# Performance work log

Measured on AMD Instinct MI355X. Metric: run time of the kernel, lower is better.

The kernel has to match this reference:

```python
import jax, jax.numpy as jnp
import numpy as np

CH = 512
COND = 1280
HEADS = 8
GROUPS = CH // 8
EPS = 1e-5


def conv2d(x, w, b, pad):
    y = jax.lax.conv_general_dilated(
        x, w, window_strides=(1, 1), padding=[(pad, pad), (pad, pad)],
        dimension_numbers=('NCHW', 'OIHW', 'NCHW'))
    return y + b[None, :, None, None]


def group_norm(x, gamma, beta, groups, eps=EPS):
    b, c, h, w = x.shape
    xg = x.reshape(b, groups, c // groups, h, w)
    mu = xg.mean(axis=(2, 3, 4), keepdims=True)
    var = xg.var(axis=(2, 3, 4), keepdims=True)
    xn = ((xg - mu) * jax.lax.rsqrt(var + eps)).reshape(b, c, h, w)
    return xn * gamma[None, :, None, None] + beta[None, :, None, None]


def setup_inputs() -> dict:
    key = jax.random.key(0)
    ks = jax.random.split(key, 20)
    s = 0.05
    inp = {
        'x': jax.random.normal(ks[0], (8, CH, 32, 32), jnp.float32),
        'conditioning': jax.random.normal(ks[1], (8, COND), jnp.float32),
        # ResBlock params
        'c1w': jax.random.normal(ks[2], (CH, CH, 3, 3), jnp.float32) * s,
        'c1b': jnp.zeros((CH,), jnp.float32),
        'g1w': jnp.ones((CH,), jnp.float32),
        'g1b': jnp.zeros((CH,), jnp.float32),
        'c2w': jax.random.normal(ks[3], (CH, CH, 3, 3), jnp.float32) * s,
        'c2b': jnp.zeros((CH,), jnp.float32),
        'g2w': jnp.ones((CH,), jnp.float32),
        'g2b': jnp.zeros((CH,), jnp.float32),
        'cpw': jax.random.normal(ks[4], (CH, COND), jnp.float32) * s,
        'cpb': jnp.zeros((CH,), jnp.float32),
        'rpw': jax.random.normal(ks[5], (CH, CH, 1, 1), jnp.float32) * s,
        'rpb': jnp.zeros((CH,), jnp.float32),
        # Attention params (1x1 convs)
        'qw': jax.random.normal(ks[6], (CH, CH, 1, 1), jnp.float32) * s,
        'qb': jnp.zeros((CH,), jnp.float32),
        'kw': jax.random.normal(ks[7], (CH, CH, 1, 1), jnp.float32) * s,
        'kb': jnp.zeros((CH,), jnp.float32),
        'vw': jax.random.normal(ks[8], (CH, CH, 1, 1), jnp.float32) * s,
        'vb': jnp.zeros((CH,), jnp.float32),
        'ow': jax.random.normal(ks[9], (CH, CH, 1, 1), jnp.float32) * s,
        'ob': jnp.zeros((CH,), jnp.float32),
    }
    return inp


def reference(x, conditioning, c1w, c1b, g1w, g1b, c2w, c2b, g2w, g2b,
              cpw, cpb, rpw, rpb, qw, qb, kw, kb, vw, vb, ow, ob):
    # --- ResBlock ---
    residual = conv2d(x, rpw, rpb, 0)
    h = conv2d(x, c1w, c1b, 1)
    h = group_norm(h, g1w, g1b, GROUPS)
    h = jax.nn.silu(h)
    h = conv2d(h, c2w, c2b, 1)
    h = group_norm(h, g2w, g2b, GROUPS)
    cond = conditioning @ cpw.T + cpb  # [B, C]
    h = h * (1.0 + cond[:, :, None, None]) + residual

    # --- SpatialSelfAttention ---
    b, c, hh, ww = h.shape
    d = c // HEADS
    scale = d ** (-0.5)
    q = conv2d(h, qw, qb, 0).reshape(b, HEADS, d, hh * ww)
    k = conv2d(h, kw, kb, 0).reshape(b, HEADS, d, hh * ww)
    v = conv2d(h, vw, vb, 0).reshape(b, HEADS, d, hh * ww)
    attn = jnp.einsum('bhdn,bhdm->bhnm', q, k) * scale  # [B,H,N,N]
    attn = jax.nn.softmax(attn, axis=-1)
    out = jnp.einsum('bhnm,bhdm->bhdn', attn, v).reshape(b, c, hh, ww)
    return conv2d(out, ow, ob, 0) + h
```

## Files before the change

### kernel.cpp

```cpp
#include <hip/hip_runtime.h>
#include <hip/hip_bf16.h>

typedef unsigned short u16;
typedef __attribute__((ext_vector_type(8))) short bf8;
typedef __attribute__((ext_vector_type(4))) short bf4;
typedef __attribute__((ext_vector_type(4))) float f32x4;

#define CH_ 512
#define NSP 1024
#define NB 8
#define CONDDIM 1280
#define NGROUP 64
#define HEADS_ 8
#define HD 64
#define PR 34
#define PPB (PR*PR)
#define QSCALE 0.18033688011112042f

#define VWAIT(N) asm volatile("s_waitcnt vmcnt(" #N ")" ::: "memory")
#define SCHEDB __builtin_amdgcn_sched_barrier(0)
#define BARRIER do { SCHEDB; __builtin_amdgcn_s_barrier(); SCHEDB; } while (0)

__device__ __forceinline__ u16 f2bf(float f) {
  union { float f; unsigned u; } v; v.f = f;
  unsigned u = v.u;
  return (u16)((u + 0x7fffu + ((u >> 16) & 1u)) >> 16);
}

__device__ __forceinline__ unsigned cvt_pk_bf16(float lo, float hi) {
  unsigned r;
  asm volatile("v_cvt_pk_bf16_f32 %0, %1, %2" : "=v"(r) : "v"(lo), "v"(hi));
  return r;
}

__device__ __forceinline__ f32x4 mfma_bf16(bf8 a, bf8 b, f32x4 c) {
  return __builtin_amdgcn_mfma_f32_16x16x32_bf16(a, b, c, 0, 0, 0);
}

__device__ __forceinline__ void gload16(const void* g, void* l) {
  __builtin_amdgcn_global_load_lds((const __attribute__((address_space(1))) void*)g,
                                   (__attribute__((address_space(3))) void*)l, 16, 0, 0);
}


__global__ __launch_bounds__(1024) void pack_x_kernel(const float* __restrict__ x, u16* __restrict__ xp) {
  __shared__ float t[32][33];
  int b = blockIdx.z;
  int c0 = blockIdx.y * 32, p0 = blockIdx.x * 32;
  int tx = threadIdx.x & 31, ty = threadIdx.x >> 5;
  t[ty][tx] = x[((size_t)b * CH_ + c0 + ty) * NSP + p0 + tx];
  __syncthreads();
  int p = p0 + ty;
  int y = p >> 5, xc = p & 31;
  xp[((size_t)b * PPB + (size_t)(y + 1) * PR + xc + 1) * CH_ + c0 + tx] = f2bf(t[tx][ty]);
}

__global__ __launch_bounds__(256) void border_zero_kernel(u16* __restrict__ a, u16* __restrict__ b) {
  int id = blockIdx.x * 256 + threadIdx.x;
  if (id >= NB * 132 * 64) return;
  int ch8 = id & 63;
  int rest = id >> 6;
  int bidx = rest % 132;
  int bb = rest / 132;
  int r, c;
  if (bidx < 34)       { r = 0;          c = bidx; }
  else if (bidx < 68)  { r = 33;         c = bidx - 34; }
  else if (bidx < 100) { r = bidx - 67;  c = 0; }
  else                 { r = bidx - 99;  c = 33; }
  size_t off = ((size_t)bb * PPB + (size_t)r * PR + c) * CH_ + ch8 * 8;
  const bf8 z = {0, 0, 0, 0, 0, 0, 0, 0};
  *(bf8*)(a + off) = z;
  *(bf8*)(b + off) = z;
}

__global__ __launch_bounds__(256) void pack_w3_kernel(const float* __restrict__ w, u16* __restrict__ wp) {
  int id = blockIdx.x * 256 + threadIdx.x;
  if (id >= 9 * 64 * CH_) return;
  int co = id & (CH_ - 1);
  int cib = (id >> 9) & 63;
  int t = id >> 15;
  int dy = t / 3, dx = t % 3;
  bf8 v;
#pragma unroll
  for (int j = 0; j < 8; j++) {
    int ci = cib * 8 + j;
    v[j] = (short)f2bf(w[(((size_t)co * CH_ + ci) * 3 + dy) * 3 + dx]);
  }
  *(bf8*)(wp + ((size_t)(t * 64 + cib) * CH_ + co) * 8) = v;
}

__global__ __launch_bounds__(256) void pack_w1_kernel(const float* __restrict__ w, u16* __restrict__ wp) {
  int id = blockIdx.x * 256 + threadIdx.x;
  if (id >= 64 * CH_) return;
  int co = id & (CH_ - 1);
  int cib = id >> 9;
  bf8 v;
#pragma unroll
  for (int j = 0; j < 8; j++) v[j] = (short)f2bf(w[(size_t)co * CH_ + cib * 8 + j]);
  *(bf8*)(wp + ((size_t)cib * CH_ + co) * 8) = v;
}

__global__ __launch_bounds__(256) void cond_kernel(const float* __restrict__ cd, const float* __restrict__ cpw,
                                                   const float* __restrict__ cpb, float* __restrict__ cond) {
  int b = blockIdx.y;
  int c = blockIdx.x * 4 + (threadIdx.x >> 6);
  int lane = threadIdx.x & 63;
  const float* wrow = cpw + (size_t)c * CONDDIM;
  const float* crow = cd + (size_t)b * CONDDIM;
  float s = 0.f;
  for (int i = lane; i < CONDDIM; i += 64) s += crow[i] * wrow[i];
#pragma unroll
  for (int m = 32; m > 0; m >>= 1) s += __shfl_xor(s, m, 64);
  if (lane == 0) cond[b * CH_ + c] = s + cpb[c];
}

template <int TAPS, int PIN, int EPI>
__global__ __launch_bounds__(256, TAPS == 9 ? 4 : 3) void conv_kernel(
    const u16* __restrict__ in, const u16* __restrict__ wp, const float* __restrict__ bias,
    float* __restrict__ outf, const float* __restrict__ addf,
    u16* __restrict__ o0, u16* __restrict__ o1, u16* __restrict__ o2,
    const float* __restrict__ b0, const float* __restrict__ b1, const float* __restrict__ b2) {
  constexpr int LDSZ = (TAPS == 9) ? (2 * 14336 + 3 * 4096) : (4 * 8192 + 4 * 4096);
  __shared__ char lds[LDSZ];
  char* ldsA = lds;
  char* ldsB = lds + ((TAPS == 9) ? 2 * 14336 : 4 * 8192);

  const int b = blockIdx.z;
  int seg = 0, coy = blockIdx.y;
  if constexpr (EPI == 5) { seg = coy >> 3; coy &= 7; }
  const int co0 = coy * 64;
  const int p0 = blockIdx.x * 128;
  const int tid = threadIdx.x;
  const int lane = tid & 63, wid = tid >> 6;
  const int wv = wid >> 1, wc = wid & 1;
  const int l15 = lane & 15, lhi = lane >> 4;

  const char* aSrc;
  if constexpr (TAPS == 9) {
    aSrc = (const char*)in + ((size_t)b * PPB + (size_t)blockIdx.x * 4 * PR) * 1024;
  } else if constexpr (PIN) {
    aSrc = (const char*)in + (size_t)b * PPB * 1024;
  } else {
    aSrc = (const char*)in + ((size_t)b * NSP + p0) * 1024;
  }
  const char* bSrc = (const char*)wp + (size_t)((EPI == 5) ? seg * 524288 : 0) + co0 * 16;

  const int pB = ((tid >> 6) * 512 + (tid & 63)) * 16;
  int pA0, pA1, pA3 = 0;
  if constexpr (TAPS == 9) {
    pA0 = ((tid >> 2) << 10) + ((tid & 3) << 4);
    pA3 = ((192 + ((tid & 127) >> 2)) << 10) + ((tid & 3) << 4);
    pA1 = 0;
  } else {
    int a0 = (tid >> 2), a1 = 64 + (tid >> 2);
    if constexpr (PIN) {
      int pp0 = p0 + a0, pp1 = p0 + a1;
      int g0 = ((pp0 >> 5) + 1) * PR + (pp0 & 31) + 1;
      int g1 = ((pp1 >> 5) + 1) * PR + (pp1 & 31) + 1;
      pA0 = (g0 << 10) + ((tid & 3) << 4);
      pA1 = (g1 << 10) + ((tid & 3) << 4);
    } else {
      pA0 = (a0 << 10) + ((tid & 3) << 4);
      pA1 = (a1 << 10) + ((tid & 3) << 4);
    }
  }

  const int aAddr = (TAPS == 9) ? ((wv * 68 + l15) * 64 + lhi * 16)
                                : ((wv * 64 + l15) * 64 + lhi * 16);
  const int bAddr = (lhi * 64 + wc * 32 + l15) * 16;

  f32x4 acc[4][2];
#pragma unroll
  for (int m = 0; m < 4; m++)
#pragma unroll
    for (int n = 0; n < 2; n++) acc[m][n] = {0.f, 0.f, 0.f, 0.f};

  if constexpr (TAPS == 9) {
    gload16(aSrc + pA0,          ldsA + (wid << 10));
    gload16(aSrc + pA0 + 65536,  ldsA + 4096 + (wid << 10));
    gload16(aSrc + pA0 + 131072, ldsA + 8192 + (wid << 10));
    gload16(aSrc + pA3,          ldsA + 12288 + ((wid & 1) << 10));
    gload16(bSrc + pB,           ldsB + (wid << 10));
    gload16(bSrc + 524288 + pB,  ldsB + 4096 + (wid << 10));
    VWAIT(1);
    BARRIER;

#define PH9(KC, T, AS) do {                                                             \
    constexpr int DT = ((T) / 3) * 34 + ((T) % 3);                                      \
    const int kcn_ = ((KC) < 15) ? (KC) + 1 : 15;                                       \
    { const int kb_ = ((T) >= 7) ? kcn_ : (KC);                                         \
      constexpr int TB = ((T) + 2) % 9;                                                 \
      gload16(bSrc + (size_t)(TB * 64 + kb_ * 4) * 8192 + pB,                           \
              ldsB + (((T) + 2) % 3) * 4096 + (wid << 10)); }                           \
    if constexpr ((T) >= 4 && (T) < 7)                                                  \
      gload16(aSrc + kcn_ * 64 + pA0 + ((T) - 4) * 65536,                               \
              ldsA + (1 - (AS)) * 14336 + ((T) - 4) * 4096 + (wid << 10));              \
    if constexpr ((T) == 7)                                                             \
      gload16(aSrc + kcn_ * 64 + pA3,                                                   \
              ldsA + (1 - (AS)) * 14336 + 12288 + ((wid & 1) << 10));                   \
    SCHEDB;                                                                             \
    bf8 af0 = *(const bf8*)(ldsA + (AS) * 14336 + DT * 64 + 0    + aAddr);              \
    bf8 af1 = *(const bf8*)(ldsA + (AS) * 14336 + DT * 64 + 1024 + aAddr);              \
    bf8 af2 = *(const bf8*)(ldsA + (AS) * 14336 + DT * 64 + 2176 + aAddr);              \
    bf8 af3 = *(const bf8*)(ldsA + (AS) * 14336 + DT * 64 + 3200 + aAddr);              \
    bf8 bq0 = *(const bf8*)(ldsB + ((T) % 3) * 4096 + 0   + bAddr);                     \
    bf8 bq1 = *(const bf8*)(ldsB + ((T) % 3) * 4096 + 256 + bAddr);                     \
    __builtin_amdgcn_s_setprio(1);                                                      \
    acc[0][0] = mfma_bf16(af0, bq0, acc[0][0]);                                         \
    acc[0][1] = mfma_bf16(af0, bq1, acc[0][1]);                                         \
    acc[1][0] = mfma_bf16(af1, bq0, acc[1][0]);                                         \
    acc[1][1] = mfma_bf16(af1, bq1, acc[1][1]);                                         \
    acc[2][0] = mfma_bf16(af2, bq0, acc[2][0]);                                         \
    acc[2][1] = mfma_bf16(af2, bq1, acc[2][1]);                                         \
    acc[3][0] = mfma_bf16(af3, bq0, acc[3][0]);                                         \
    acc[3][1] = mfma_bf16(af3, bq1, acc[3][1]);                                         \
    __builtin_amdgcn_s_setprio(0);                                                      \
    if constexpr ((T) >= 4 && (T) <= 7) { VWAIT(2); } else { VWAIT(1); }                \
    BARRIER;                                                                            \
  } while (0)

    for (int kc2 = 0; kc2 < 8; kc2++) {
      PH9(kc2 * 2, 0, 0); PH9(kc2 * 2, 1, 0); PH9(kc2 * 2, 2, 0);
      PH9(kc2 * 2, 3, 0); PH9(kc2 * 2, 4, 0); PH9(kc2 * 2, 5, 0);
      PH9(kc2 * 2, 6, 0); PH9(kc2 * 2, 7, 0); PH9(kc2 * 2, 8, 0);
      PH9(kc2 * 2 + 1, 0, 1); PH9(kc2 * 2 + 1, 1, 1); PH9(kc2 * 2 + 1, 2, 1);
      PH9(kc2 * 2 + 1, 3, 1); PH9(kc2 * 2 + 1, 4, 1); PH9(kc2 * 2 + 1, 5, 1);
      PH9(kc2 * 2 + 1, 6, 1); PH9(kc2 * 2 + 1, 7, 1); PH9(kc2 * 2 + 1, 8, 1);
    }
#undef PH9
  } else {
    gload16(aSrc + pA0,         ldsA + (wid << 10));
    gload16(aSrc + pA1,         ldsA + 4096 + (wid << 10));
    gload16(bSrc + pB,          ldsB + (wid << 10));
    gload16(aSrc + 64 + pA0,    ldsA + 8192 + (wid << 10));
    gload16(aSrc + 64 + pA1,    ldsA + 8192 + 4096 + (wid << 10));
    gload16(bSrc + 32768 + pB,  ldsB + 4096 + (wid << 10));
    VWAIT(3);
    BARRIER;

#define PH1(KC, S) do {                                                                 \
    constexpr int S2 = ((S) + 2) & 3;                                                   \
    const int kcn_ = ((KC) + 2 < 16) ? (KC) + 2 : 15;                                   \
    gload16(bSrc + (size_t)kcn_ * 32768 + pB, ldsB + S2 * 4096 + (wid << 10));          \
    gload16(aSrc + kcn_ * 64 + pA0, ldsA + S2 * 8192 + (wid << 10));                    \
    gload16(aSrc + kcn_ * 64 + pA1, ldsA + S2 * 8192 + 4096 + (wid << 10));             \
    SCHEDB;                                                                             \
    bf8 af0 = *(const bf8*)(ldsA + (S) * 8192 + 0    + aAddr);                          \
    bf8 af1 = *(const bf8*)(ldsA + (S) * 8192 + 1024 + aAddr);                          \
    bf8 af2 = *(const bf8*)(ldsA + (S) * 8192 + 2048 + aAddr);                          \
    bf8 af3 = *(const bf8*)(ldsA + (S) * 8192 + 3072 + aAddr);                          \
    bf8 bq0 = *(const bf8*)(ldsB + (S) * 4096 + 0   + bAddr);                           \
    bf8 bq1 = *(const bf8*)(ldsB + (S) * 4096 + 256 + bAddr);                           \
    __builtin_amdgcn_s_setprio(1);                                                      \
    acc[0][0] = mfma_bf16(af0, bq0, acc[0][0]);                                         \
    acc[0][1] = mfma_bf16(af0, bq1, acc[0][1]);                                         \
    acc[1][0] = mfma_bf16(af1, bq0, acc[1][0]);                                         \
    acc[1][1] = mfma_bf16(af1, bq1, acc[1][1]);                                         \
    acc[2][0] = mfma_bf16(af2, bq0, acc[2][0]);                                         \
    acc[2][1] = mfma_bf16(af2, bq1, acc[2][1]);                                         \
    acc[3][0] = mfma_bf16(af3, bq0, acc[3][0]);                                         \
    acc[3][1] = mfma_bf16(af3, bq1, acc[3][1]);                                         \
    __builtin_amdgcn_s_setprio(0);                                                      \
    VWAIT(3);                                                                           \
    BARRIER;                                                                            \
  } while (0)

    for (int kc4 = 0; kc4 < 4; kc4++) {
      PH1(kc4 * 4 + 0, 0); PH1(kc4 * 4 + 1, 1); PH1(kc4 * 4 + 2, 2); PH1(kc4 * 4 + 3, 3);
    }
#undef PH1
  }

  VWAIT(0);

#pragma unroll
  for (int m = 0; m < 4; m++) {
    int pbase = p0 + wv * 64 + m * 16 + lhi * 4;
#pragma unroll
    for (int n = 0; n < 2; n++) {
      int co = co0 + wc * 32 + n * 16 + l15;
      if constexpr (EPI == 0) {
        float bv = bias[co];
#pragma unroll
        for (int r = 0; r < 4; r++)
          outf[((size_t)b * NSP + pbase + r) * CH_ + co] = acc[m][n][r] + bv;
      } else if constexpr (EPI == 2) {
        float bv = bias[co];
        f32x4 v;
#pragma unroll
        for (int r = 0; r < 4; r++)
          v[r] = acc[m][n][r] + bv + addf[((size_t)b * NSP + pbase + r) * CH_ + co];
        *(f32x4*)(outf + ((size_t)b * CH_ + co) * NSP + pbase) = v;
      } else {
        if (seg == 0) {
          float bv = b0[co];
#pragma unroll
          for (int r = 0; r < 4; r++)
            o0[((size_t)b * NSP + pbase + r) * CH_ + co] = f2bf((acc[m][n][r] + bv) * QSCALE);
        } else if (seg == 1) {
          float bv = b1[co];
#pragma unroll
          for (int r = 0; r < 4; r++)
            o1[((size_t)b * NSP + pbase + r) * CH_ + co] = f2bf(acc[m][n][r] + bv);
        } else {
          float bv = b2[co];
          union { bf4 v; unsigned long long u; } pk4;
#pragma unroll
          for (int r = 0; r < 4; r++) pk4.v[r] = (short)f2bf(acc[m][n][r] + bv);
          *(unsigned long long*)(o2 + ((size_t)b * CH_ + co) * NSP + pbase) = pk4.u;
        }
      }
    }
  }
}

template <int MODE>
__global__ __launch_bounds__(256) void gn_kernel(
    const float* __restrict__ in, const float* __restrict__ gw, const float* __restrict__ gb,
    const float* __restrict__ cond, const float* __restrict__ resid,
    float* __restrict__ outf, u16* __restrict__ outb) {
  int b = blockIdx.y, g = blockIdx.x;
  int tid = threadIdx.x;
  int c = g * 8 + (tid & 7);
  int prow = tid >> 3;
  const float* base = in + (size_t)b * NSP * CH_ + c;
  float v[32];
  float s = 0.f, ss = 0.f;
#pragma unroll
  for (int i = 0; i < 32; i++) {
    v[i] = base[(size_t)(prow + i * 32) * CH_];
    s += v[i]; ss += v[i] * v[i];
  }
  __shared__ float rs[256], rss[256];
  rs[tid] = s; rss[tid] = ss;
  __syncthreads();
  for (int off = 128; off > 0; off >>= 1) {
    if (tid < off) { rs[tid] += rs[tid + off]; rss[tid] += rss[tid + off]; }
    __syncthreads();
  }
  float mean = rs[0] * (1.f / 8192.f);
  float var = rss[0] * (1.f / 8192.f) - mean * mean;
  float inv = rsqrtf(var + 1e-5f);
  float gamma = gw[c], beta = gb[c];
  float cm = 0.f;
  if (MODE == 1) cm = 1.f + cond[b * CH_ + c];
#pragma unroll
  for (int i = 0; i < 32; i++) {
    int p = prow + i * 32;
    float y = (v[i] - mean) * inv * gamma + beta;
    if (MODE == 0) {
      float sg = 1.f / (1.f + __expf(-y));
      int yy = p >> 5, xc = p & 31;
      outb[((size_t)b * PPB + (size_t)(yy + 1) * PR + xc + 1) * CH_ + c] = f2bf(y * sg);
    } else {
      size_t idx = ((size_t)b * NSP + p) * CH_ + c;
      float z = y * cm + resid[idx];
      outf[idx] = z;
      outb[idx] = f2bf(z);
    }
  }
}

__global__ __launch_bounds__(256) void attn_kernel(const u16* __restrict__ q, const u16* __restrict__ k,
                                                   const u16* __restrict__ vT, u16* __restrict__ ao) {
  int bid = blockIdx.x;
  int swz = (bid & 7) * 64 + (bid >> 3);
  int b = swz >> 6;
  int head = (swz >> 3) & 7;
  int qt = swz & 7;
  int tid = threadIdx.x, lane = tid & 63, wid = tid >> 6;
  int l15 = lane & 15, lhi = lane >> 4;
  int cb = head * HD;
  int q0 = qt * 128 + wid * 32;

  const char* qp = (const char*)(q + (size_t)b * NSP * CH_ + cb);
  const char* kp = (const char*)(k + (size_t)b * NSP * CH_ + cb);
  const char* vp = (const char*)(vT + ((size_t)b * CH_ + cb) * NSP);

  __shared__ u16 Ksh[3][64 * 64];
  __shared__ u16 Vsh[3][64 * 64];

  bf8 aq[2][2];
#pragma unroll
  for (int qh = 0; qh < 2; qh++)
#pragma unroll
    for (int ks = 0; ks < 2; ks++)
      aq[qh][ks] = *(const bf8*)(qp + ((size_t)(q0 + qh * 16 + l15) * CH_ + ks * 32 + lhi * 8) * 2);

  f32x4 o[2][4];
  float mrow[2], lpart[2];
#pragma unroll
  for (int qh = 0; qh < 2; qh++) {
    mrow[qh] = -1e30f; lpart[qh] = 0.f;
#pragma unroll
    for (int n = 0; n < 4; n++) o[qh][n] = {0.f, 0.f, 0.f, 0.f};
  }

  auto stage = [&](int kt, int buf) {
#pragma unroll
    for (int t = 0; t < 2; t++) {
      int i = wid * 2 + t;
      int chunk = i * 64 + lane;
      int r = chunk >> 3, c = chunk & 7;
      gload16(kp + (size_t)(kt * 64 + r) * 1024 + (size_t)((c ^ (r & 7)) * 16),
              (char*)Ksh[buf] + i * 1024);
    }
#pragma unroll
    for (int t = 0; t < 2; t++) {
      int i = wid * 2 + t;
      int chunk = i * 64 + lane;
      int r = chunk >> 3, c = chunk & 7;
      gload16(vp + (size_t)r * 2048 + (size_t)(kt * 128) + (size_t)((c ^ (r & 7)) * 16),
              (char*)Vsh[buf] + i * 1024);
    }
  };

  stage(0, 0);
  stage(1, 1);

  int cB = 0, sB = 2;
  for (int kt = 0; kt < 16; ++kt) {
    if (kt < 15) { VWAIT(4); } else { VWAIT(0); }
    BARRIER;
    if (kt < 14) stage(kt + 2, sB);
    const char* Kb = (const char*)Ksh[0] + cB * 8192;
    const char* Vb = (const char*)Vsh[0] + cB * 8192;

    f32x4 sacc[2][4];
#pragma unroll
    for (int qh = 0; qh < 2; qh++)
#pragma unroll
      for (int kf = 0; kf < 4; kf++) sacc[qh][kf] = {0.f, 0.f, 0.f, 0.f};

#pragma unroll
    for (int kf = 0; kf < 4; kf++) {
      bf8 ak[2];
#pragma unroll
      for (int ks = 0; ks < 2; ks++)
        ak[ks] = *(const bf8*)(Kb + (size_t)(kf * 16 + l15) * 128 + (((ks * 4 + lhi) ^ (l15 & 7)) * 16));
#pragma unroll
      for (int qh = 0; qh < 2; qh++)
#pragma unroll
        for (int ks = 0; ks < 2; ks++)
          sacc[qh][kf] = mfma_bf16(ak[ks], aq[qh][ks], sacc[qh][kf]);
    }

    unsigned pk[2][4][2];
#pragma unroll
    for (int qh = 0; qh < 2; qh++) {
      float m0 = fmaxf(fmaxf(sacc[qh][0][0], sacc[qh][0][1]), fmaxf(sacc[qh][0][2], sacc[qh][0][3]));
      float m1 = fmaxf(fmaxf(sacc[qh][1][0], sacc[qh][1][1]), fmaxf(sacc[qh][1][2], sacc[qh][1][3]));
      float m2 = fmaxf(fmaxf(sacc[qh][2][0], sacc[qh][2][1]), fmaxf(sacc[qh][2][2], sacc[qh][2][3]));
      float m3 = fmaxf(fmaxf(sacc[qh][3][0], sacc[qh][3][1]), fmaxf(sacc[qh][3][2], sacc[qh][3][3]));
      float pml = fmaxf(fmaxf(m0, m1), fmaxf(m2, m3));
      if (__any(pml > mrow[qh] + 8.f)) {
        float pm = fmaxf(pml, __shfl_xor(pml, 16, 64));
        pm = fmaxf(pm, __shfl_xor(pm, 32, 64));
        float mn = fmaxf(mrow[qh], pm);
        float corr = exp2f(mrow[qh] - mn);
        mrow[qh] = mn;
        lpart[qh] *= corr;
        float corr_o[4];
#pragma unroll
        for (int r = 0; r < 4; r++) corr_o[r] = __shfl(corr, lhi * 4 + r, 64);
#pragma unroll
        for (int n = 0; n < 4; n++)
#pragma unroll
          for (int r = 0; r < 4; r++) o[qh][n][r] *= corr_o[r];
      }
      float rsum = 0.f;
#pragma unroll
      for (int kf = 0; kf < 4; kf++) {
        f32x4 pv;
#pragma unroll
        for (int r = 0; r < 4; r++) {
          pv[r] = exp2f(sacc[qh][kf][r] - mrow[qh]);
          rsum += pv[r];
        }
        pk[qh][kf][0] = cvt_pk_bf16(pv[0], pv[1]);
        pk[qh][kf][1] = cvt_pk_bf16(pv[2], pv[3]);
      }
      lpart[qh] += rsum;
    }

#pragma unroll
    for (int g = 0; g < 2; g++) {
      union { bf8 v8; unsigned u[4]; } ap[2];
#pragma unroll
      for (int qh = 0; qh < 2; qh++) {
        ap[qh].u[0] = pk[qh][2 * g][0];
        ap[qh].u[1] = pk[qh][2 * g][1];
        ap[qh].u[2] = pk[qh][2 * g + 1][0];
        ap[qh].u[3] = pk[qh][2 * g + 1][1];
      }
#pragma unroll
      for (int nf2 = 0; nf2 < 4; nf2++) {
        int row = nf2 * 16 + l15;
        int c0 = 4 * g + (lhi >> 1);
        union { bf8 v8; bf4 v4[2]; } bv;
        bv.v4[0] = *(const bf4*)(Vb + (size_t)row * 128 + ((c0 ^ (l15 & 7)) * 16) + (lhi & 1) * 8);
        bv.v4[1] = *(const bf4*)(Vb + (size_t)row * 128 + (((c0 + 2) ^ (l15 & 7)) * 16) + (lhi & 1) * 8);
#pragma unroll
        for (int qh = 0; qh < 2; qh++)
          o[qh][nf2] = mfma_bf16(ap[qh].v8, bv.v8, o[qh][nf2]);
      }
    }

    cB = (cB == 2) ? 0 : cB + 1;
    sB = (sB == 2) ? 0 : sB + 1;
  }

#pragma unroll
  for (int qh = 0; qh < 2; qh++) {
    float lrow = lpart[qh];
    lrow += __shfl_xor(lrow, 16, 64);
    lrow += __shfl_xor(lrow, 32, 64);
    float linv[4];
#pragma unroll
    for (int r = 0; r < 4; r++) linv[r] = 1.f / __shfl(lrow, lhi * 4 + r, 64);
#pragma unroll
    for (int nf2 = 0; nf2 < 4; nf2++)
#pragma unroll
      for (int r = 0; r < 4; r++) {
        float val = o[qh][nf2][r] * linv[r];
        ao[((size_t)b * NSP + q0 + qh * 16 + lhi * 4 + r) * CH_ + cb + nf2 * 16 + l15] = f2bf(val);
      }
  }
}


extern "C" void kernel_launch(void* const* d_in, const int* in_sizes, int n_in,
                              void* d_out, int out_size, void* d_ws, size_t ws_size,
                              hipStream_t stream) {
  const float* x    = (const float*)d_in[0];
  const float* cnd  = (const float*)d_in[1];
  const float* c1w  = (const float*)d_in[2];
  const float* c1b  = (const float*)d_in[3];
  const float* g1w  = (const float*)d_in[4];
  const float* g1b  = (const float*)d_in[5];
  const float* c2w  = (const float*)d_in[6];
  const float* c2b  = (const float*)d_in[7];
  const float* g2w  = (const float*)d_in[8];
  const float* g2b  = (const float*)d_in[9];
  const float* cpw  = (const float*)d_in[10];
  const float* cpb  = (const float*)d_in[11];
  const float* rpw  = (const float*)d_in[12];
  const float* rpb  = (const float*)d_in[13];
  const float* qw   = (const float*)d_in[14];
  const float* qb   = (const float*)d_in[15];
  const float* kw   = (const float*)d_in[16];
  const float* kb   = (const float*)d_in[17];
  const float* vw   = (const float*)d_in[18];
  const float* vb   = (const float*)d_in[19];
  const float* ow   = (const float*)d_in[20];
  const float* ob   = (const float*)d_in[21];
  float* out = (float*)d_out;

  char* ws = (char*)d_ws;
  size_t off = 0;
  auto alloc = [&](size_t bytes) -> char* {
    char* p = ws + off;
    off = (off + bytes + 255) & ~(size_t)255;
    return p;
  };
  const size_t ACT_F = (size_t)NB * NSP * CH_ * 4;
  const size_t ACT_B = (size_t)NB * NSP * CH_ * 2;
  const size_t PAD_B = (size_t)NB * PPB * CH_ * 2;

  u16* xp    = (u16*)alloc(PAD_B);
  u16* h1p   = (u16*)alloc(PAD_B);
  u16* w1p   = (u16*)alloc((size_t)9 * CH_ * CH_ * 2);
  u16* w2p   = (u16*)alloc((size_t)9 * CH_ * CH_ * 2);
  u16* wrp   = (u16*)alloc((size_t)CH_ * CH_ * 2);
  u16* wqkv  = (u16*)alloc((size_t)3 * CH_ * CH_ * 2);
  u16* wop   = (u16*)alloc((size_t)CH_ * CH_ * 2);
  float* cndv = (float*)alloc((size_t)NB * CH_ * 4);
  float* resid = (float*)alloc(ACT_F);
  float* h12  = (float*)alloc(ACT_F);
  u16* hb    = (u16*)alloc(ACT_B);
  u16* qbuf  = (u16*)alloc(ACT_B);
  u16* kbuf  = (u16*)alloc(ACT_B);
  u16* vTb   = (u16*)alloc(ACT_B);
  u16* aob   = (u16*)alloc(ACT_B);
  if (off > ws_size) return;

  dim3 tgrid(NSP / 32, CH_ / 32, NB);
  border_zero_kernel<<<(NB * 132 * 64 + 255) / 256, 256, 0, stream>>>(xp, h1p);
  pack_x_kernel<<<tgrid, 1024, 0, stream>>>(x, xp);
  pack_w3_kernel<<<(9 * 64 * CH_ + 255) / 256, 256, 0, stream>>>(c1w, w1p);
  pack_w3_kernel<<<(9 * 64 * CH_ + 255) / 256, 256, 0, stream>>>(c2w, w2p);
  pack_w1_kernel<<<(64 * CH_) / 256, 256, 0, stream>>>(rpw, wrp);
  pack_w1_kernel<<<(64 * CH_) / 256, 256, 0, stream>>>(qw, wqkv);
  pack_w1_kernel<<<(64 * CH_) / 256, 256, 0, stream>>>(kw, wqkv + (size_t)CH_ * CH_);
  pack_w1_kernel<<<(64 * CH_) / 256, 256, 0, stream>>>(vw, wqkv + (size_t)2 * CH_ * CH_);
  pack_w1_kernel<<<(64 * CH_) / 256, 256, 0, stream>>>(ow, wop);
  cond_kernel<<<dim3(CH_ / 4, NB), 256, 0, stream>>>(cnd, cpw, cpb, cndv);

  dim3 ggrid(NSP / 128, CH_ / 64, NB);
  dim3 qgrid(NSP / 128, 3 * CH_ / 64, NB);
  conv_kernel<9, 1, 0><<<ggrid, 256, 0, stream>>>(xp, w1p, c1b, h12, nullptr,
                                                  nullptr, nullptr, nullptr, nullptr, nullptr, nullptr);
  conv_kernel<1, 1, 0><<<ggrid, 256, 0, stream>>>(xp, wrp, rpb, resid, nullptr,
                                                  nullptr, nullptr, nullptr, nullptr, nullptr, nullptr);
  gn_kernel<0><<<dim3(NGROUP, NB), 256, 0, stream>>>(h12, g1w, g1b, nullptr, nullptr, nullptr, h1p);
  conv_kernel<9, 1, 0><<<ggrid, 256, 0, stream>>>(h1p, w2p, c2b, h12, nullptr,
                                                  nullptr, nullptr, nullptr, nullptr, nullptr, nullptr);
  gn_kernel<1><<<dim3(NGROUP, NB), 256, 0, stream>>>(h12, g2w, g2b, cndv, resid, h12, hb);
  conv_kernel<1, 0, 5><<<qgrid, 256, 0, stream>>>(hb, wqkv, nullptr, nullptr, nullptr,
                                                  qbuf, kbuf, vTb, qb, kb, vb);
  attn_kernel<<<512, 256, 0, stream>>>(qbuf, kbuf, vTb, aob);
  conv_kernel<1, 0, 2><<<ggrid, 256, 0, stream>>>(aob, wop, ob, out, h12,
                                                  nullptr, nullptr, nullptr, nullptr, nullptr, nullptr);
}
```

Baseline: 265.2 us.

## Restructure 3x3 conv pipeline per row, software-pipeline attention, batch weight packing

The 3x3 conv main loop now stages the weights for a whole kernel row of three taps per phase, with double-buffered B tiles. This cuts the number of barriers per K chunk from nine to three, at the cost of more LDS and lower occupancy (launch bounds drop from 4 to 3). The attention kernel is software-pipelined so the next tile's QK^T overlaps the current softmax and PV, and the V layout is permuted so each lane reads one 16-byte vector instead of two 8-byte ones. The seven weight-packing launches are merged into two using a grid y dimension.

```diff
diff --git a/kernel.cpp b/kernel.cpp
--- a/kernel.cpp
+++ b/kernel.cpp
@@ -2,6 +2,7 @@
 #include <hip/hip_bf16.h>
 
 typedef unsigned short u16;
+typedef unsigned long long u64;
 typedef __attribute__((ext_vector_type(8))) short bf8;
 typedef __attribute__((ext_vector_type(4))) short bf4;
 typedef __attribute__((ext_vector_type(4))) float f32x4;
@@ -73,9 +74,12 @@
   *(bf8*)(b + off) = z;
 }
 
-__global__ __launch_bounds__(256) void pack_w3_kernel(const float* __restrict__ w, u16* __restrict__ wp) {
+__global__ __launch_bounds__(256) void pack_w3_kernel(const float* __restrict__ wA, const float* __restrict__ wB,
+                                                      u16* __restrict__ dA, u16* __restrict__ dB) {
   int id = blockIdx.x * 256 + threadIdx.x;
   if (id >= 9 * 64 * CH_) return;
+  const float* w = blockIdx.y ? wB : wA;
+  u16* wp = blockIdx.y ? dB : dA;
   int co = id & (CH_ - 1);
   int cib = (id >> 9) & 63;
   int t = id >> 15;
@@ -89,9 +93,21 @@
   *(bf8*)(wp + ((size_t)(t * 64 + cib) * CH_ + co) * 8) = v;
 }
 
-__global__ __launch_bounds__(256) void pack_w1_kernel(const float* __restrict__ w, u16* __restrict__ wp) {
+__global__ __launch_bounds__(256) void pack_w1_kernel(
+    const float* __restrict__ s0, const float* __restrict__ s1, const float* __restrict__ s2,
+    const float* __restrict__ s3, const float* __restrict__ s4,
+    u16* __restrict__ d0, u16* __restrict__ d1, u16* __restrict__ d2,
+    u16* __restrict__ d3, u16* __restrict__ d4) {
   int id = blockIdx.x * 256 + threadIdx.x;
   if (id >= 64 * CH_) return;
+  const float* w; u16* wp;
+  switch (blockIdx.y) {
+    case 0: w = s0; wp = d0; break;
+    case 1: w = s1; wp = d1; break;
+    case 2: w = s2; wp = d2; break;
+    case 3: w = s3; wp = d3; break;
+    default: w = s4; wp = d4; break;
+  }
   int co = id & (CH_ - 1);
   int cib = id >> 9;
   bf8 v;
@@ -115,12 +131,12 @@
 }
 
 template <int TAPS, int PIN, int EPI>
-__global__ __launch_bounds__(256, TAPS == 9 ? 4 : 3) void conv_kernel(
+__global__ __launch_bounds__(256, 3) void conv_kernel(
     const u16* __restrict__ in, const u16* __restrict__ wp, const float* __restrict__ bias,
     float* __restrict__ outf, const float* __restrict__ addf,
     u16* __restrict__ o0, u16* __restrict__ o1, u16* __restrict__ o2,
     const float* __restrict__ b0, const float* __restrict__ b1, const float* __restrict__ b2) {
-  constexpr int LDSZ = (TAPS == 9) ? (2 * 14336 + 3 * 4096) : (4 * 8192 + 4 * 4096);
+  constexpr int LDSZ = (TAPS == 9) ? (2 * 14336 + 2 * 12288) : (4 * 8192 + 4 * 4096);
   __shared__ char lds[LDSZ];
   char* ldsA = lds;
   char* ldsB = lds + ((TAPS == 9) ? 2 * 14336 : 4 * 8192);
@@ -182,52 +198,63 @@
     gload16(aSrc + pA3,          ldsA + 12288 + ((wid & 1) << 10));
     gload16(bSrc + pB,           ldsB + (wid << 10));
     gload16(bSrc + 524288 + pB,  ldsB + 4096 + (wid << 10));
-    VWAIT(1);
+    gload16(bSrc + 1048576 + pB, ldsB + 8192 + (wid << 10));
+    VWAIT(0);
     BARRIER;
 
-#define PH9(KC, T, AS) do {                                                             \
-    constexpr int DT = ((T) / 3) * 34 + ((T) % 3);                                      \
+#define PH3(KC, T, AS, H) do {                                                          \
     const int kcn_ = ((KC) < 15) ? (KC) + 1 : 15;                                       \
-    { const int kb_ = ((T) >= 7) ? kcn_ : (KC);                                         \
-      constexpr int TB = ((T) + 2) % 9;                                                 \
-      gload16(bSrc + (size_t)(TB * 64 + kb_ * 4) * 8192 + pB,                           \
-              ldsB + (((T) + 2) % 3) * 4096 + (wid << 10)); }                           \
-    if constexpr ((T) >= 4 && (T) < 7)                                                  \
-      gload16(aSrc + kcn_ * 64 + pA0 + ((T) - 4) * 65536,                               \
-              ldsA + (1 - (AS)) * 14336 + ((T) - 4) * 4096 + (wid << 10));              \
-    if constexpr ((T) == 7)                                                             \
-      gload16(aSrc + kcn_ * 64 + pA3,                                                   \
-              ldsA + (1 - (AS)) * 14336 + 12288 + ((wid & 1) << 10));                   \
+    { const int kb_ = ((T) == 2) ? kcn_ : (KC);                                         \
+      const int tn_ = 3 * (((T) + 1) % 3);                                              \
+      gload16(bSrc + (size_t)((tn_ + 0) * 64 + kb_ * 4) * 8192 + pB,                    \
+              ldsB + (1 - (H)) * 12288 + (wid << 10));                                  \
+      gload16(bSrc + (size_t)((tn_ + 1) * 64 + kb_ * 4) * 8192 + pB,                    \
+              ldsB + (1 - (H)) * 12288 + 4096 + (wid << 10));                           \
+      gload16(bSrc + (size_t)((tn_ + 2) * 64 + kb_ * 4) * 8192 + pB,                    \
+              ldsB + (1 - (H)) * 12288 + 8192 + (wid << 10)); }                         \
+    if constexpr ((T) == 0) {                                                           \
+      gload16(aSrc + kcn_ * 64 + pA0,         ldsA + (1-(AS))*14336 + (wid << 10));     \
+      gload16(aSrc + kcn_ * 64 + pA0 + 65536, ldsA + (1-(AS))*14336 + 4096 + (wid<<10));\
+    }                                                                                   \
+    if constexpr ((T) == 1)                                                             \
+      gload16(aSrc + kcn_ * 64 + pA0 + 131072, ldsA + (1-(AS))*14336 + 8192 + (wid<<10));\
+    if constexpr ((T) == 2)                                                             \
+      gload16(aSrc + kcn_ * 64 + pA3, ldsA + (1-(AS))*14336 + 12288 + ((wid&1)<<10));   \
     SCHEDB;                                                                             \
-    bf8 af0 = *(const bf8*)(ldsA + (AS) * 14336 + DT * 64 + 0    + aAddr);              \
-    bf8 af1 = *(const bf8*)(ldsA + (AS) * 14336 + DT * 64 + 1024 + aAddr);              \
-    bf8 af2 = *(const bf8*)(ldsA + (AS) * 14336 + DT * 64 + 2176 + aAddr);              \
-    bf8 af3 = *(const bf8*)(ldsA + (AS) * 14336 + DT * 64 + 3200 + aAddr);              \
-    bf8 bq0 = *(const bf8*)(ldsB + ((T) % 3) * 4096 + 0   + bAddr);                     \
-    bf8 bq1 = *(const bf8*)(ldsB + ((T) % 3) * 4096 + 256 + bAddr);                     \
-    __builtin_amdgcn_s_setprio(1);                                                      \
-    acc[0][0] = mfma_bf16(af0, bq0, acc[0][0]);                                         \
-    acc[0][1] = mfma_bf16(af0, bq1, acc[0][1]);                                         \
-    acc[1][0] = mfma_bf16(af1, bq0, acc[1][0]);                                         \
-    acc[1][1] = mfma_bf16(af1, bq1, acc[1][1]);                                         \
-    acc[2][0] = mfma_bf16(af2, bq0, acc[2][0]);                                         \
-    acc[2][1] = mfma_bf16(af2, bq1, acc[2][1]);                                         \
-    acc[3][0] = mfma_bf16(af3, bq0, acc[3][0]);                                         \
-    acc[3][1] = mfma_bf16(af3, bq1, acc[3][1]);                                         \
-    __builtin_amdgcn_s_setprio(0);                                                      \
-    if constexpr ((T) >= 4 && (T) <= 7) { VWAIT(2); } else { VWAIT(1); }                \
+    {                                                                                   \
+      const char* Ab_ = ldsA + (AS) * 14336;                                            \
+      const char* Bb_ = ldsB + (H) * 12288;                                             \
+      bf8 af_[3][4], bq_[3][2];                                                         \
+      _Pragma("unroll")                                                                 \
+      for (int tt = 0; tt < 3; tt++) {                                                  \
+        const int DT_ = (T) * 34 + tt;                                                  \
+        af_[tt][0] = *(const bf8*)(Ab_ + DT_ * 64 + 0    + aAddr);                      \
+        af_[tt][1] = *(const bf8*)(Ab_ + DT_ * 64 + 1024 + aAddr);                      \
+        af_[tt][2] = *(const bf8*)(Ab_ + DT_ * 64 + 2176 + aAddr);                      \
+        af_[tt][3] = *(const bf8*)(Ab_ + DT_ * 64 + 3200 + aAddr);                      \
+        bq_[tt][0] = *(const bf8*)(Bb_ + tt * 4096 + 0   + bAddr);                      \
+        bq_[tt][1] = *(const bf8*)(Bb_ + tt * 4096 + 256 + bAddr);                      \
+      }                                                                                 \
+      __builtin_amdgcn_s_setprio(1);                                                    \
+      _Pragma("unroll")                                                                 \
+      for (int tt = 0; tt < 3; tt++)                                                    \
+        _Pragma("unroll")                                                               \
+        for (int m = 0; m < 4; m++) {                                                   \
+          acc[m][0] = mfma_bf16(af_[tt][m], bq_[tt][0], acc[m][0]);                     \
+          acc[m][1] = mfma_bf16(af_[tt][m], bq_[tt][1], acc[m][1]);                     \
+        }                                                                               \
+      __builtin_amdgcn_s_setprio(0);                                                    \
+    }                                                                                   \
+    if constexpr ((T) == 0) { VWAIT(2); } else if constexpr ((T) == 1) { VWAIT(1); }    \
+    else { VWAIT(0); }                                                                  \
     BARRIER;                                                                            \
   } while (0)
 
     for (int kc2 = 0; kc2 < 8; kc2++) {
-      PH9(kc2 * 2, 0, 0); PH9(kc2 * 2, 1, 0); PH9(kc2 * 2, 2, 0);
-      PH9(kc2 * 2, 3, 0); PH9(kc2 * 2, 4, 0); PH9(kc2 * 2, 5, 0);
-      PH9(kc2 * 2, 6, 0); PH9(kc2 * 2, 7, 0); PH9(kc2 * 2, 8, 0);
-      PH9(kc2 * 2 + 1, 0, 1); PH9(kc2 * 2 + 1, 1, 1); PH9(kc2 * 2 + 1, 2, 1);
-      PH9(kc2 * 2 + 1, 3, 1); PH9(kc2 * 2 + 1, 4, 1); PH9(kc2 * 2 + 1, 5, 1);
-      PH9(kc2 * 2 + 1, 6, 1); PH9(kc2 * 2 + 1, 7, 1); PH9(kc2 * 2 + 1, 8, 1);
-    }
-#undef PH9
+      PH3(kc2 * 2,     0, 0, 0); PH3(kc2 * 2,     1, 0, 1); PH3(kc2 * 2,     2, 0, 0);
+      PH3(kc2 * 2 + 1, 0, 1, 1); PH3(kc2 * 2 + 1, 1, 1, 0); PH3(kc2 * 2 + 1, 2, 1, 1);
+    }
+#undef PH3
   } else {
     gload16(aSrc + pA0,         ldsA + (wid << 10));
     gload16(aSrc + pA1,         ldsA + 4096 + (wid << 10));
@@ -304,10 +331,11 @@
             o1[((size_t)b * NSP + pbase + r) * CH_ + co] = f2bf(acc[m][n][r] + bv);
         } else {
           float bv = b2[co];
-          union { bf4 v; unsigned long long u; } pk4;
+          union { bf4 v; u64 u; } pk4;
 #pragma unroll
           for (int r = 0; r < 4; r++) pk4.v[r] = (short)f2bf(acc[m][n][r] + bv);
-          *(unsigned long long*)(o2 + ((size_t)b * CH_ + co) * NSP + pbase) = pk4.u;
+          int np = (pbase & ~31) | ((pbase & 12) << 1) | ((pbase & 16) >> 2);
+          *(u64*)(o2 + ((size_t)b * CH_ + co) * NSP + np) = pk4.u;
         }
       }
     }
@@ -361,8 +389,8 @@
   }
 }
 
-__global__ __launch_bounds__(256) void attn_kernel(const u16* __restrict__ q, const u16* __restrict__ k,
-                                                   const u16* __restrict__ vT, u16* __restrict__ ao) {
+__global__ __launch_bounds__(256, 2) void attn_kernel(const u16* __restrict__ q, const u16* __restrict__ k,
+                                                      const u16* __restrict__ vT, u16* __restrict__ ao) {
   int bid = blockIdx.x;
   int swz = (bid & 7) * 64 + (bid >> 3);
   int b = swz >> 6;
@@ -415,23 +443,12 @@
     }
   };
 
-  stage(0, 0);
-  stage(1, 1);
-
-  int cB = 0, sB = 2;
-  for (int kt = 0; kt < 16; ++kt) {
-    if (kt < 15) { VWAIT(4); } else { VWAIT(0); }
-    BARRIER;
-    if (kt < 14) stage(kt + 2, sB);
-    const char* Kb = (const char*)Ksh[0] + cB * 8192;
-    const char* Vb = (const char*)Vsh[0] + cB * 8192;
-
-    f32x4 sacc[2][4];
+  auto qk = [&](int buf, f32x4 (&sacc)[2][4]) {
+    const char* Kb = (const char*)Ksh[0] + buf * 8192;
 #pragma unroll
     for (int qh = 0; qh < 2; qh++)
 #pragma unroll
       for (int kf = 0; kf < 4; kf++) sacc[qh][kf] = {0.f, 0.f, 0.f, 0.f};
-
 #pragma unroll
     for (int kf = 0; kf < 4; kf++) {
       bf8 ak[2];
@@ -444,7 +461,10 @@
         for (int ks = 0; ks < 2; ks++)
           sacc[qh][kf] = mfma_bf16(ak[ks], aq[qh][ks], sacc[qh][kf]);
     }
-
+  };
+
+  auto smpv = [&](int buf, f32x4 (&sacc)[2][4]) {
+    const char* Vb = (const char*)Vsh[0] + buf * 8192;
     unsigned pk[2][4][2];
 #pragma unroll
     for (int qh = 0; qh < 2; qh++) {
@@ -482,7 +502,6 @@
       }
       lpart[qh] += rsum;
     }
-
 #pragma unroll
     for (int g = 0; g < 2; g++) {
       union { bf8 v8; unsigned u[4]; } ap[2];
@@ -496,18 +515,50 @@
 #pragma unroll
       for (int nf2 = 0; nf2 < 4; nf2++) {
         int row = nf2 * 16 + l15;
-        int c0 = 4 * g + (lhi >> 1);
-        union { bf8 v8; bf4 v4[2]; } bv;
-        bv.v4[0] = *(const bf4*)(Vb + (size_t)row * 128 + ((c0 ^ (l15 & 7)) * 16) + (lhi & 1) * 8);
-        bv.v4[1] = *(const bf4*)(Vb + (size_t)row * 128 + (((c0 + 2) ^ (l15 & 7)) * 16) + (lhi & 1) * 8);
+        bf8 bv8 = *(const bf8*)(Vb + (size_t)row * 128 + (((4 * g + lhi) ^ (l15 & 7)) * 16));
 #pragma unroll
         for (int qh = 0; qh < 2; qh++)
-          o[qh][nf2] = mfma_bf16(ap[qh].v8, bv.v8, o[qh][nf2]);
+          o[qh][nf2] = mfma_bf16(ap[qh].v8, bv8, o[qh][nf2]);
       }
     }
-
-    cB = (cB == 2) ? 0 : cB + 1;
-    sB = (sB == 2) ? 0 : sB + 1;
+  };
+
+  stage(0, 0);
+  stage(1, 1);
+  VWAIT(4);
+  BARRIER;
+
+  f32x4 saccA[2][4], saccB[2][4];
+  qk(0, saccA);
+
+  int bc = 0;
+  for (int kt2 = 0; kt2 < 8; kt2++) {
+    {
+      int kt = 2 * kt2;
+      int bn = (bc == 2) ? 0 : bc + 1;
+      int bs = (bn == 2) ? 0 : bn + 1;
+      VWAIT(0);
+      BARRIER;
+      qk(bn, saccB);
+      if (kt < 14) stage(kt + 2, bs);
+      smpv(bc, saccA);
+      bc = bn;
+    }
+    {
+      int kt = 2 * kt2 + 1;
+      if (kt < 15) {
+        int bn = (bc == 2) ? 0 : bc + 1;
+        int bs = (bn == 2) ? 0 : bn + 1;
+        VWAIT(0);
+        BARRIER;
+        qk(bn, saccA);
+        if (kt < 14) stage(kt + 2, bs);
+        smpv(bc, saccB);
+        bc = bn;
+      } else {
+        smpv(bc, saccB);
+      }
+    }
   }
 
 #pragma unroll
@@ -587,13 +638,10 @@
   dim3 tgrid(NSP / 32, CH_ / 32, NB);
   border_zero_kernel<<<(NB * 132 * 64 + 255) / 256, 256, 0, stream>>>(xp, h1p);
   pack_x_kernel<<<tgrid, 1024, 0, stream>>>(x, xp);
-  pack_w3_kernel<<<(9 * 64 * CH_ + 255) / 256, 256, 0, stream>>>(c1w, w1p);
-  pack_w3_kernel<<<(9 * 64 * CH_ + 255) / 256, 256, 0, stream>>>(c2w, w2p);
-  pack_w1_kernel<<<(64 * CH_) / 256, 256, 0, stream>>>(rpw, wrp);
-  pack_w1_kernel<<<(64 * CH_) / 256, 256, 0, stream>>>(qw, wqkv);
-  pack_w1_kernel<<<(64 * CH_) / 256, 256, 0, stream>>>(kw, wqkv + (size_t)CH_ * CH_);
-  pack_w1_kernel<<<(64 * CH_) / 256, 256, 0, stream>>>(vw, wqkv + (size_t)2 * CH_ * CH_);
-  pack_w1_kernel<<<(64 * CH_) / 256, 256, 0, stream>>>(ow, wop);
+  pack_w3_kernel<<<dim3((9 * 64 * CH_ + 255) / 256, 2), 256, 0, stream>>>(c1w, c2w, w1p, w2p);
+  pack_w1_kernel<<<dim3((64 * CH_) / 256, 5), 256, 0, stream>>>(
+      rpw, qw, kw, vw, ow,
+      wrp, wqkv, wqkv + (size_t)CH_ * CH_, wqkv + (size_t)2 * CH_ * CH_, wop);
   cond_kernel<<<dim3(CH_ / 4, NB), 256, 0, stream>>>(cnd, cpw, cpb, cndv);
 
   dim3 ggrid(NSP / 128, CH_ / 64, NB);
```

Measured after the change: 255.0 us. 3.9% less time.
